# Performance work log

Hardware: AMD Instinct MI355X
Metric: run time of the kernel (lower is better)

## Reference

```python
import jax, jax.numpy as jnp
import numpy as np

NX, NY = 512, 512
FNUM, GNUM = 120, 120
NA = 1.35
WAVELENGTH = NX * NA / 100.0  # chosen so normalized period = 100
N_LIQUID = 1.44
M_RED = 0.25
LOW_LIGHT_THRES = 1e-3
SRC_STEEP = 8.0
RESIST_STEEP = 30.0
RESIST_INT = 0.225
DOSES = (0.98, 1.0, 1.02)
SRC_GRID = 13

X1 = NX // 2 - FNUM; X2 = NX // 2 + FNUM + 1
Y1 = NY // 2 - GNUM; Y2 = NY // 2 + GNUM + 1
_PER_X = NX / (WAVELENGTH / NA)
_PER_Y = NY / (WAVELENGTH / NA)
NORM_SPEC = _PER_X * _PER_Y
DFMDG = 1.0 / NORM_SPEC
_fm = (np.arange(X1, X2) - NX // 2) / _PER_X
_gm = (np.arange(Y1, Y2) - NY // 2) / _PER_Y
_FM, _GM = np.meshgrid(_fm, _gm)  # 'xy' indexing, shape [2*GNUM+1, 2*FNUM+1]
FM = jnp.asarray(_FM, jnp.float32)
GM = jnp.asarray(_GM, jnp.float32)


def cal_pupil(fg2):
    # obliquity factor; pupil phase is identically zero in this module
    num = 1.0 - (M_RED ** 2) * (NA ** 2) * fg2
    den = 1.0 - (NA / N_LIQUID) ** 2 * fg2
    return jnp.sqrt(jnp.sqrt(num / den))


def setup_inputs() -> dict:
    key = jax.random.key(0)
    g = np.linspace(-1.0, 1.0, SRC_GRID, dtype=np.float32)
    fxg, fyg = np.meshgrid(g, g)
    r = np.sqrt(fxg ** 2 + fyg ** 2)
    data = ((r >= 0.6) & (r <= 0.9)).astype(np.float32)  # annular source
    # sigmoid activation init: +1 where lit, -1 elsewhere (zeros, set 2 where data>0.5, sub 1)
    params = 2.0 * data - 1.0
    mask_value = jax.random.uniform(key, (NY, NX), jnp.float32)
    return {
        "mask_value": mask_value,
        "source_params": jnp.asarray(params, jnp.float32),
        "source_fx": jnp.asarray(fxg.reshape(-1), jnp.float32),
        "source_fy": jnp.asarray(fyg.reshape(-1), jnp.float32),
    }


def _forward(mask_value, source_params, source_fx, source_fy):
    # source activation + low-light pruning (masked_select expressed as zero-weighting)
    val = jax.nn.sigmoid(SRC_STEEP * source_params).reshape(-1)  # [S]
    valid = val >= LOW_LIGHT_THRES
    w = jnp.where(valid, val, 0.0)
    weight = jnp.sum(w)

    # normalization intensity (detached in the original)
    fxy2 = source_fx ** 2 + source_fy ** 2
    obl = cal_pupil(jnp.where(valid, fxy2, 0.0))
    norm_I = jax.lax.stop_gradient(
        N_LIQUID * DFMDG ** 2 * jnp.sum(w * (NORM_SPEC * obl) ** 2) / weight
    )

    # shifted pupil per source point over the mask frequency window
    F = FM[None, :, :] + source_fx[:, None, None]  # [S, Gy, Gx]
    G = GM[None, :, :] + source_fy[:, None, None]
    rho2 = F * F + G * G                            # == mask_fg2m + 2(fx*fm+fy*gm) + fxy2
    vmask = rho2 <= 1.0
    pupil = jnp.where(vmask, cal_pupil(jnp.where(vmask, rho2, 0.0)), 0.0)  # [S, Gy, Gx]

    S = w.shape[0]
    Is, Rs = [], []
    for d in DOSES:
        fv = jnp.fft.fftshift(jnp.fft.fft2(jnp.fft.ifftshift(mask_value * d)))
        win = fv[Y1:Y2, X1:X2]                      # [Gy, Gx] complex
        tempH = win[None, :, :] * pupil.astype(jnp.complex64)  # masked spectrum*pupil
        e = jnp.zeros((S, NY, NX), jnp.complex64).at[:, Y1:Y2, X1:X2].set(tempH)
        AA = jnp.fft.fftshift(jnp.fft.ifft2(e), axes=(-2, -1))
        I2 = AA.real ** 2 + AA.imag ** 2            # |AA * conj(AA)|
        intensity = jnp.einsum('s,syx->yx', w, I2) / weight / norm_I
        Is.append(intensity)
        Rs.append(jax.nn.sigmoid(RESIST_STEEP * (intensity - RESIST_INT)))
    # [2, 3, NY, NX]: [0] = aerial intensity per dose, [1] = resist image per dose
    return jnp.stack([jnp.stack(Is), jnp.stack(Rs)])


def reference(mask_value, source_params, source_fx, source_fy):
    return _forward(mask_value, source_params, source_fx, source_fy)
```

## Files before the change

### kernel.cpp

```cpp
#include <hip/hip_runtime.h>
#include <hip/hip_bf16.h>
#include <hip/hip_fp16.h>


#define SPLIT 8

static const size_t O_TW   = 4096;
static const size_t O_ACC  = 8192;
static const size_t ACC_BYTES = (size_t)SPLIT * 512 * 512 * 4;
static const size_t O_WIN  = O_ACC + ACC_BYTES;
static const size_t O_R1   = O_WIN + 464896;
static const size_t O_T2   = O_R1 + 987136;
static const size_t SLOT_BYTES = (size_t)512 * 244 * 4;

__device__ inline float2 cadd(float2 a, float2 b){ return make_float2(a.x+b.x, a.y+b.y); }
__device__ inline float2 csub(float2 a, float2 b){ return make_float2(a.x-b.x, a.y-b.y); }
__device__ inline float2 cmul(float2 a, float2 b){
  return make_float2(fmaf(a.x, b.x, -(a.y*b.y)), fmaf(a.x, b.y, a.y*b.x));
}
__device__ inline float2 twsgn(float2 t, int S) {
  return make_float2(t.x, (S > 0) ? t.y : -t.y);
}

template<int S, bool ZTOP>
__device__ inline void dft8(float2 v[8]) {
  const float sg = (float)S;
  const float C7 = 0.7071067811865476f;
  float2 t0, t1, t2, t3, t4, t5, t6, t7;
  if (ZTOP) {
    t0 = v[0]; t4 = v[0];
    t1 = v[1]; t5 = v[1];
    t2 = v[2]; t6 = v[2];
    t3 = v[3]; t7 = v[3];
  } else {
    t0=cadd(v[0],v[4]); t4=csub(v[0],v[4]);
    t1=cadd(v[1],v[5]); t5=csub(v[1],v[5]);
    t2=cadd(v[2],v[6]); t6=csub(v[2],v[6]);
    t3=cadd(v[3],v[7]); t7=csub(v[3],v[7]);
  }
  t5 = make_float2(C7*(t5.x - sg*t5.y), C7*(t5.y + sg*t5.x));
  t6 = make_float2(-sg*t6.y, sg*t6.x);
  t7 = make_float2(C7*(-t7.x - sg*t7.y), C7*(sg*t7.x - t7.y));
  float2 u0=cadd(t0,t2), u2=csub(t0,t2);
  float2 u1=cadd(t1,t3), u3=csub(t1,t3);
  u3 = make_float2(-sg*u3.y, sg*u3.x);
  float2 u4=cadd(t4,t6), u6=csub(t4,t6);
  float2 u5=cadd(t5,t7), u7=csub(t5,t7);
  u7 = make_float2(-sg*u7.y, sg*u7.x);
  v[0]=cadd(u0,u1); v[4]=csub(u0,u1);
  v[2]=cadd(u2,u3); v[6]=csub(u2,u3);
  v[1]=cadd(u4,u5); v[5]=csub(u4,u5);
  v[3]=cadd(u6,u7); v[7]=csub(u6,u7);
}

template<int S, bool ZTOP>
__device__ inline void wfft512(float2 v[8], int lane, float2* xch,
                               const float2* twt) {
  const int p2 = lane & 7, u0 = lane >> 3;
  dft8<S, ZTOP>(v);
  { float2 t1 = twsgn(twt[lane], S), acc = t1;
    v[1] = cmul(v[1], acc);
    #pragma unroll
    for (int u = 2; u < 8; u++) { acc = cmul(acc, t1); v[u] = cmul(v[u], acc); } }
  __builtin_amdgcn_wave_barrier();
  #pragma unroll
  for (int u = 0; u < 8; u++) xch[u*68 + p2*8 + u0] = v[u];
  __builtin_amdgcn_wave_barrier();
  { const float4* rp = (const float4*)(xch + u0*68 + p2*8);
    #pragma unroll
    for (int q = 0; q < 4; q++) {
      float4 t = rp[q];
      v[2*q]   = make_float2(t.x, t.y);
      v[2*q+1] = make_float2(t.z, t.w);
    } }
  dft8<S, false>(v);
  { float2 t1 = twsgn(twt[p2 << 3], S), acc = t1;
    v[1] = cmul(v[1], acc);
    #pragma unroll
    for (int u = 2; u < 8; u++) { acc = cmul(acc, t1); v[u] = cmul(v[u], acc); } }
  __builtin_amdgcn_wave_barrier();
  #pragma unroll
  for (int u = 0; u < 8; u++) xch[u*68 + lane] = v[u];
  __builtin_amdgcn_wave_barrier();
  { const float4* rp = (const float4*)(xch + p2*68 + u0*8);
    #pragma unroll
    for (int q = 0; q < 4; q++) {
      float4 t = rp[q];
      v[2*q]   = make_float2(t.x, t.y);
      v[2*q+1] = make_float2(t.z, t.w);
    } }
  dft8<S, false>(v);
}

__global__ void __launch_bounds__(256) k_setup(const float* prm, const float* sfx,
                                               const float* sfy, char* ws) {
  __shared__ float sw[169], sx[169], sy[169], scw[169];
  __shared__ double so[169];
  __shared__ int skeep[169];
  int t = threadIdx.x;
  if (t < 169) {
    float p = prm[t];
    float val = 1.f / (1.f + __expf(-8.f * p));
    float w = (val >= 0.001f) ? val : 0.f;
    double o = 0.0; float fx = 0.f, fy = 0.f;
    if (w > 0.f) {
      fx = sfx[t]; fy = sfy[t];
      double f2 = (double)fx*(double)fx + (double)fy*(double)fy;
      o = (double)w * sqrt((1.0 - 0.11390625 * f2) / (1.0 - 0.87890625 * f2));
    }
    sw[t] = w; so[t] = o; sx[t] = fx; sy[t] = fy;
  }
  float2* gtw = (float2*)(ws + O_TW);
  for (int k = t; k < 512; k += 256) {
    double a = 6.283185307179586476925286766559 * (double)k / 512.0;
    gtw[k] = make_float2((float)cos(a), (float)sin(a));
  }
  if (t < 241) ((float*)ws)[768 + t] = (float)(((double)(t - 120)) / 100.0);
  __syncthreads();
  if (t < 169) {
    float w = sw[t];
    int keep = 0; float cw = w;
    if (w > 0.f) {
      float fx = sx[t], fy = sy[t];
      int pr = -1;
      for (int s2 = 0; s2 < 169; s2++) {
        if (sw[s2] > 0.f && fabsf(sx[s2] + fx) < 1e-5f
                         && fabsf(sy[s2] + fy) < 1e-5f) { pr = s2; break; }
      }
      if (pr < 0 || pr == t) keep = 1;
      else if (pr > t) { keep = 1; cw = w + sw[pr]; }
    }
    skeep[t] = keep; scw[t] = cw;
  }
  __syncthreads();
  if (t == 0) {
    float* wsf = (float*)ws; int* wsi = (int*)ws;
    double Sden = 0.0; int c = 0;
    for (int s = 0; s < 169; s++) {
      Sden += so[s];
      if (skeep[s]) { wsf[64+c] = scw[s]; wsf[320+c] = sx[s]; wsf[576+c] = sy[s]; c++; }
    }
    wsi[0] = c;
    wsf[1] = (float)(1.0 / (262144.0 * 1.44 * Sden));
  }
}

__global__ void __launch_bounds__(256, 6) k_b1(const float* mask, const char* wsb,
                                               float2* R1t) {
  int lane = threadIdx.x & 63, wv = threadIdx.x >> 6;
  int y = blockIdx.x * 4 + wv;
  __shared__ __align__(16) float2 lds[4*544];
  __shared__ __align__(16) float2 twt[512];
  ((float4*)twt)[threadIdx.x] = ((const float4*)(wsb + O_TW))[threadIdx.x];
  __syncthreads();
  float2 v[8];
  #pragma unroll
  for (int q = 0; q < 8; q++) v[q] = make_float2(mask[y*512 + 64*q + lane], 0.f);
  wfft512<-1, false>(v, lane, lds + wv*544, twt);
  #pragma unroll
  for (int u = 0; u < 8; u++) {
    int k = (lane>>3) + 8*(lane&7) + 64*u;
    int beta = (k >= 392) ? (k - 392) : ((k <= 120) ? (k + 120) : -1);
    if (beta >= 0) R1t[beta*512 + y] = v[u];
  }
}

__global__ void __launch_bounds__(256, 6) k_b2(const float2* R1t, const char* wsb,
                                               float2* Wg) {
  int lane = threadIdx.x & 63, wv = threadIdx.x >> 6;
  int j = blockIdx.x * 4 + wv;
  __shared__ __align__(16) float2 lds[4*544];
  __shared__ __align__(16) float2 twt[512];
  ((float4*)twt)[threadIdx.x] = ((const float4*)(wsb + O_TW))[threadIdx.x];
  __syncthreads();
  float2 v[8];
  #pragma unroll
  for (int q = 0; q < 8; q++)
    v[q] = (j < 241) ? R1t[j*512 + 64*q + lane] : make_float2(0.f, 0.f);
  wfft512<-1, false>(v, lane, lds + wv*544, twt);
  if (j < 241) {
    #pragma unroll
    for (int u = 0; u < 8; u++) {
      int k = (lane>>3) + 8*(lane&7) + 64*u;
      int alpha = (k >= 392) ? (k - 392) : ((k <= 120) ? (k + 120) : -1);
      if (alpha >= 0) Wg[alpha*241 + j] = v[u];
    }
  }
}

__global__ void __launch_bounds__(256, 7) k_c1(const float2* Wg, const char* wsb,
                                               int base, __half2* T2) {
  const int*   cnt = (const int*)wsb;
  const float* wsf = (const float*)wsb;
  const float* FMt = (const float*)(wsb + 3072);
  int sic  = blockIdx.x / 31;
  int tile = blockIdx.x % 31;
  int slot = base + sic;
  if (slot >= *cnt) return;
  __shared__ __align__(16) float2 lds[4*544];
  __shared__ __align__(16) float2 twt[512];
  ((float4*)twt)[threadIdx.x] = ((const float4*)(wsb + O_TW))[threadIdx.x];
  __syncthreads();
  float fx = wsf[320 + slot], fy = wsf[576 + slot];
  float sqw = __fsqrt_rn(wsf[64 + slot]) * 0.001953125f;
  int lane = threadIdx.x & 63, wv = threadIdx.x >> 6;
  float2* xch = lds + wv*544;
  #pragma unroll
  for (int ph = 0; ph < 2; ph++) {
    int alpha = tile*8 + ph*4 + wv;
    bool arow = (alpha < 241);
    float Gf = __fadd_rn(arow ? FMt[alpha] : 0.f, fy);
    float g2 = __fmul_rn(Gf, Gf);
    bool active = arow && (g2 <= 1.0f);
    float2 v[8];
    #pragma unroll
    for (int q = 0; q < 8; q++) v[q] = make_float2(0.f, 0.f);
    if (active) {
      #pragma unroll
      for (int q = 0; q < 4; q++) {
        int n = 64*q + lane;
        if (n < 241) {
          float Ff = __fadd_rn(FMt[n], fx);
          float r2 = __fadd_rn(__fmul_rn(Ff, Ff), g2);
          if (r2 <= 1.0f) {
            float num = fmaf(-0.11390625f, r2, 1.0f);
            float den = fmaf(-0.87890625f, r2, 1.0f);
            float P = __fsqrt_rn(__fsqrt_rn(__fdividef(num, den))) * sqw;
            float2 Wv = Wg[alpha*241 + n];
            v[q] = make_float2(P * Wv.x, P * Wv.y);
          }
        }
      }
      wfft512<1, true>(v, lane, xch, twt);
    }
    #pragma unroll
    for (int u = 0; u < 8; u++) {
      int xx = (lane>>3) + 8*(lane&7) + 64*u;
      xch[xx] = v[u];
    }
    __syncthreads();
    int colb = tile*8 + ph*4;
    if (colb < 244) {
      #pragma unroll
      for (int r = 0; r < 2; r++) {
        int x = (int)threadIdx.x + 256*r;
        union { __half2 h[4]; float4 f; } u;
        #pragma unroll
        for (int wvi = 0; wvi < 4; wvi++) {
          float2 a = lds[wvi*544 + x];
          u.h[wvi] = __floats2half2_rn(a.x, a.y);
        }
        *(float4*)(T2 + ((size_t)sic*512 + x)*244 + colb) = u.f;
      }
    }
    __syncthreads();
  }
}

__global__ void __launch_bounds__(256, 7) k_c2(const __half2* T2, const char* wsb,
                                               int base, int CH, int first,
                                               float* accbuf) {
  const int* cnt = (const int*)wsb;
  int part = blockIdx.x & (SPLIT-1);
  int xg   = blockIdx.x >> 3;
  int lane = threadIdx.x & 63, wv = threadIdx.x >> 6;
  int x = xg*4 + wv;
  __shared__ __align__(16) float2 lds[4*544];
  __shared__ __align__(16) float2 twt[512];
  ((float4*)twt)[threadIdx.x] = ((const float4*)(wsb + O_TW))[threadIdx.x];
  __syncthreads();
  float2* xch = lds + wv*544;
  int count = *cnt;
  float av[8] = {0.f,0.f,0.f,0.f,0.f,0.f,0.f,0.f};
  int sic = part;
  bool act = (sic < CH) && (base + sic < count);
  __half2 pv[4] = {{0.f,0.f},{0.f,0.f},{0.f,0.f},{0.f,0.f}};
  if (act) {
    const __half2* row = T2 + ((size_t)sic*512 + x)*244;
    #pragma unroll
    for (int q = 0; q < 4; q++) {
      int n = 64*q + lane;
      pv[q] = (n < 241) ? row[n] : __half2{0.f, 0.f};
    }
  }
  while (act) {
    float2 v[8];
    #pragma unroll
    for (int q = 0; q < 4; q++) { float2 f = __half22float2(pv[q]); v[q] = f; }
    #pragma unroll
    for (int q = 4; q < 8; q++) v[q] = make_float2(0.f, 0.f);
    int nsic = sic + SPLIT;
    act = (nsic < CH) && (base + nsic < count);
    if (act) {
      const __half2* row = T2 + ((size_t)nsic*512 + x)*244;
      #pragma unroll
      for (int q = 0; q < 4; q++) {
        int n = 64*q + lane;
        pv[q] = (n < 241) ? row[n] : __half2{0.f, 0.f};
      }
    }
    wfft512<1, true>(v, lane, xch, twt);
    #pragma unroll
    for (int u = 0; u < 8; u++)
      av[u] += fmaf(v[u].x, v[u].x, v[u].y*v[u].y);
    sic = nsic;
  }
  float* a = accbuf + ((size_t)part << 18) + (size_t)x * 512;
  int y0 = (lane>>3) + 8*(lane&7);
  if (first) {
    #pragma unroll
    for (int u = 0; u < 8; u++) a[y0 + 64*u] = av[u];
  } else {
    #pragma unroll
    for (int u = 0; u < 8; u++) a[y0 + 64*u] += av[u];
  }
}

__global__ void __launch_bounds__(256) k_final(const float* acc, const char* wsb,
                                               float* out) {
  __shared__ float tile[64][65];
  const float* wsf = (const float*)wsb;
  float scale = wsf[1];
  int x0 = (blockIdx.x & 7) * 64, y0 = (blockIdx.x >> 3) * 64;
  int j = threadIdx.x & 63, i0 = threadIdx.x >> 6;
  #pragma unroll
  for (int k = 0; k < 16; k++) {
    int i = i0 + 4*k;
    const float* ap = acc + (size_t)(x0 + i)*512 + y0 + j;
    float s = 0.f;
    #pragma unroll
    for (int p = 0; p < SPLIT; p++) s += ap[(size_t)p << 18];
    tile[i][j] = s;
  }
  __syncthreads();
  const float dd[3] = {0.9604f, 1.0f, 1.0404f};
  #pragma unroll
  for (int k = 0; k < 16; k++) {
    int yy = i0 + 4*k;
    float I = scale * tile[j][yy];
    int o = (y0 + yy)*512 + x0 + j;
    #pragma unroll
    for (int d = 0; d < 3; d++) {
      float Ik = dd[d] * I;
      out[(size_t)d*262144 + o] = Ik;
      out[(size_t)(3+d)*262144 + o] = 1.f / (1.f + __expf(-30.f*(Ik - 0.225f)));
    }
  }
}

extern "C" void kernel_launch(void* const* d_in, const int* in_sizes, int n_in,
                              void* d_out, int out_size, void* d_ws, size_t ws_size,
                              hipStream_t stream) {
  (void)in_sizes; (void)n_in; (void)out_size;
  const float* mask = (const float*)d_in[0];
  const float* prm  = (const float*)d_in[1];
  const float* sfx  = (const float*)d_in[2];
  const float* sfy  = (const float*)d_in[3];
  float* out = (float*)d_out;
  char*  ws  = (char*)d_ws;

  float*   acc = (float*)(ws + O_ACC);
  float2*  Wg  = (float2*)(ws + O_WIN);
  float2*  R1t = (float2*)(ws + O_R1);
  __half2* T2  = (__half2*)(ws + O_T2);

  k_setup<<<dim3(1),   dim3(256), 0, stream>>>(prm, sfx, sfy, ws);
  k_b1  <<<dim3(128), dim3(256), 0, stream>>>(mask, (const char*)ws, R1t);
  k_b2  <<<dim3(61),  dim3(256), 0, stream>>>(R1t, (const char*)ws, Wg);

  size_t avail = (ws_size > O_T2) ? (ws_size - O_T2) : 0;
  int CH = (int)(avail / SLOT_BYTES);
  if (CH > 169) CH = 169;
  if (CH < 1)   CH = 1;
  for (int base = 0; base < 169; base += CH) {
    k_c1<<<dim3((unsigned)(CH*31)),  dim3(256), 0, stream>>>(Wg, (const char*)ws, base, T2);
    k_c2<<<dim3(128*SPLIT),          dim3(256), 0, stream>>>(T2, (const char*)ws, base, CH,
                                                             (base == 0) ? 1 : 0, acc);
  }
  k_final<<<dim3(64), dim3(256), 0, stream>>>(acc, (const char*)ws, out);
}
```

Baseline: 138.3 us.

## Fuse all stages into one persistent kernel with software grid barriers

Replaces the chain of setup, row FFT, column FFT, per-source pupil FFT, accumulate and finalize kernels with a single persistent kernel of 512 blocks. Stages are separated by an atomic-counter grid barrier, which removes launch overhead and inter-kernel gaps. The c2 stage now maps one block per column with four waves splitting sources (SPLIT reduced to 4). The CH chunking that depended on workspace size is dropped, so all source slots must fit in the workspace at once. Correctness depends on all 512 blocks being co-resident; if they are not, the spin barrier can deadlock. Also, fewer blocks work in the early stages and c2 parallelism changes.

```diff
diff --git a/kernel.cpp b/kernel.cpp
--- a/kernel.cpp
+++ b/kernel.cpp
@@ -3,9 +3,10 @@
 #include <hip/hip_fp16.h>
 
 
-#define SPLIT 8
-
-static const size_t O_TW   = 4096;
+#define NBLK 512
+#define SPLIT 4
+
+static const size_t O_BAR  = 2048;
 static const size_t O_ACC  = 8192;
 static const size_t ACC_BYTES = (size_t)SPLIT * 512 * 512 * 4;
 static const size_t O_WIN  = O_ACC + ACC_BYTES;
@@ -20,6 +21,19 @@
 }
 __device__ inline float2 twsgn(float2 t, int S) {
   return make_float2(t.x, (S > 0) ? t.y : -t.y);
+}
+
+__device__ inline void gridbar(int* cnt, int gen) {
+  __syncthreads();
+  if (threadIdx.x == 0) {
+    __threadfence();
+    atomicAdd(cnt, 1);
+    int target = (gen + 1) * NBLK;
+    while (__hip_atomic_load(cnt, __ATOMIC_ACQUIRE, __HIP_MEMORY_SCOPE_AGENT) < target)
+      __builtin_amdgcn_s_sleep(2);
+    __threadfence();
+  }
+  __syncthreads();
 }
 
 template<int S, bool ZTOP>
@@ -92,258 +106,244 @@
   dft8<S, false>(v);
 }
 
-__global__ void __launch_bounds__(256) k_setup(const float* prm, const float* sfx,
-                                               const float* sfy, char* ws) {
-  __shared__ float sw[169], sx[169], sy[169], scw[169];
-  __shared__ double so[169];
-  __shared__ int skeep[169];
-  int t = threadIdx.x;
-  if (t < 169) {
-    float p = prm[t];
-    float val = 1.f / (1.f + __expf(-8.f * p));
-    float w = (val >= 0.001f) ? val : 0.f;
-    double o = 0.0; float fx = 0.f, fy = 0.f;
-    if (w > 0.f) {
-      fx = sfx[t]; fy = sfy[t];
-      double f2 = (double)fx*(double)fx + (double)fy*(double)fy;
-      o = (double)w * sqrt((1.0 - 0.11390625 * f2) / (1.0 - 0.87890625 * f2));
-    }
-    sw[t] = w; so[t] = o; sx[t] = fx; sy[t] = fy;
-  }
-  float2* gtw = (float2*)(ws + O_TW);
+#define ARENA_BYTES (4096 + 17408 + 1024)
+
+__global__ void __launch_bounds__(256, 2)
+k_fused(const float* __restrict__ mask, const float* __restrict__ prm,
+        const float* __restrict__ sfx, const float* __restrict__ sfy,
+        char* __restrict__ ws, float* __restrict__ out) {
+  __shared__ __align__(16) char arena[ARENA_BYTES];
+  float2* twt = (float2*)arena;
+  float2* lds = (float2*)(arena + 4096);
+  float*  FMt = (float*)(arena + 4096 + 17408);
+  int*    bar = (int*)(ws + O_BAR);
+  float*  wsf = (float*)ws;
+  int t = threadIdx.x, lane = t & 63, wv = t >> 6, b = blockIdx.x;
+
+  float*   acc = (float*)(ws + O_ACC);
+  float2*  Wg  = (float2*)(ws + O_WIN);
+  float2*  R1t = (float2*)(ws + O_R1);
+  __half2* T2  = (__half2*)(ws + O_T2);
+
   for (int k = t; k < 512; k += 256) {
     double a = 6.283185307179586476925286766559 * (double)k / 512.0;
-    gtw[k] = make_float2((float)cos(a), (float)sin(a));
-  }
-  if (t < 241) ((float*)ws)[768 + t] = (float)(((double)(t - 120)) / 100.0);
-  __syncthreads();
-  if (t < 169) {
-    float w = sw[t];
-    int keep = 0; float cw = w;
-    if (w > 0.f) {
-      float fx = sx[t], fy = sy[t];
-      int pr = -1;
-      for (int s2 = 0; s2 < 169; s2++) {
-        if (sw[s2] > 0.f && fabsf(sx[s2] + fx) < 1e-5f
-                         && fabsf(sy[s2] + fy) < 1e-5f) { pr = s2; break; }
-      }
-      if (pr < 0 || pr == t) keep = 1;
-      else if (pr > t) { keep = 1; cw = w + sw[pr]; }
-    }
-    skeep[t] = keep; scw[t] = cw;
-  }
-  __syncthreads();
-  if (t == 0) {
-    float* wsf = (float*)ws; int* wsi = (int*)ws;
-    double Sden = 0.0; int c = 0;
-    for (int s = 0; s < 169; s++) {
-      Sden += so[s];
-      if (skeep[s]) { wsf[64+c] = scw[s]; wsf[320+c] = sx[s]; wsf[576+c] = sy[s]; c++; }
-    }
-    wsi[0] = c;
-    wsf[1] = (float)(1.0 / (262144.0 * 1.44 * Sden));
-  }
-}
-
-__global__ void __launch_bounds__(256, 6) k_b1(const float* mask, const char* wsb,
-                                               float2* R1t) {
-  int lane = threadIdx.x & 63, wv = threadIdx.x >> 6;
-  int y = blockIdx.x * 4 + wv;
-  __shared__ __align__(16) float2 lds[4*544];
-  __shared__ __align__(16) float2 twt[512];
-  ((float4*)twt)[threadIdx.x] = ((const float4*)(wsb + O_TW))[threadIdx.x];
-  __syncthreads();
-  float2 v[8];
-  #pragma unroll
-  for (int q = 0; q < 8; q++) v[q] = make_float2(mask[y*512 + 64*q + lane], 0.f);
-  wfft512<-1, false>(v, lane, lds + wv*544, twt);
-  #pragma unroll
-  for (int u = 0; u < 8; u++) {
-    int k = (lane>>3) + 8*(lane&7) + 64*u;
-    int beta = (k >= 392) ? (k - 392) : ((k <= 120) ? (k + 120) : -1);
-    if (beta >= 0) R1t[beta*512 + y] = v[u];
-  }
-}
-
-__global__ void __launch_bounds__(256, 6) k_b2(const float2* R1t, const char* wsb,
-                                               float2* Wg) {
-  int lane = threadIdx.x & 63, wv = threadIdx.x >> 6;
-  int j = blockIdx.x * 4 + wv;
-  __shared__ __align__(16) float2 lds[4*544];
-  __shared__ __align__(16) float2 twt[512];
-  ((float4*)twt)[threadIdx.x] = ((const float4*)(wsb + O_TW))[threadIdx.x];
-  __syncthreads();
-  float2 v[8];
-  #pragma unroll
-  for (int q = 0; q < 8; q++)
-    v[q] = (j < 241) ? R1t[j*512 + 64*q + lane] : make_float2(0.f, 0.f);
-  wfft512<-1, false>(v, lane, lds + wv*544, twt);
-  if (j < 241) {
+    twt[k] = make_float2((float)cos(a), (float)sin(a));
+  }
+  if (t < 241) FMt[t] = (float)(((double)(t - 120)) / 100.0);
+
+  if (b == 0) {
+    float*  sw   = (float*)(arena + 4096);
+    float*  sx_  = sw + 192;
+    float*  sy_  = sx_ + 192;
+    float*  scw  = sy_ + 192;
+    double* so   = (double*)(arena + 4096 + 3072);
+    int*    skp  = (int*)(arena + 4096 + 3072 + 1408);
+    if (t < 169) {
+      float p = prm[t];
+      float val = 1.f / (1.f + __expf(-8.f * p));
+      float w = (val >= 0.001f) ? val : 0.f;
+      double o = 0.0; float fx = 0.f, fy = 0.f;
+      if (w > 0.f) {
+        fx = sfx[t]; fy = sfy[t];
+        double f2 = (double)fx*(double)fx + (double)fy*(double)fy;
+        o = (double)w * sqrt((1.0 - 0.11390625 * f2) / (1.0 - 0.87890625 * f2));
+      }
+      sw[t] = w; so[t] = o; sx_[t] = fx; sy_[t] = fy;
+    }
+    __syncthreads();
+    if (t < 169) {
+      float w = sw[t];
+      int keep = 0; float cw = w;
+      if (w > 0.f) {
+        float fx = sx_[t], fy = sy_[t];
+        int pr = -1;
+        for (int s2 = 0; s2 < 169; s2++) {
+          if (sw[s2] > 0.f && fabsf(sx_[s2] + fx) < 1e-5f
+                           && fabsf(sy_[s2] + fy) < 1e-5f) { pr = s2; break; }
+        }
+        if (pr < 0 || pr == t) keep = 1;
+        else if (pr > t) { keep = 1; cw = w + sw[pr]; }
+      }
+      skp[t] = keep; scw[t] = cw;
+    }
+    __syncthreads();
+    if (t == 0) {
+      double Sden = 0.0; int c = 0;
+      for (int s = 0; s < 169; s++) {
+        Sden += so[s];
+        if (skp[s]) { wsf[64+c] = scw[s]; wsf[320+c] = sx_[s]; wsf[576+c] = sy_[s]; c++; }
+      }
+      ((int*)ws)[0] = c;
+      wsf[1] = (float)(1.0 / (262144.0 * 1.44 * Sden));
+    }
+  }
+  gridbar(bar, 0);
+
+  if (b < 128) {
+    int y = b * 4 + wv;
+    float2 v[8];
+    #pragma unroll
+    for (int q = 0; q < 8; q++) v[q] = make_float2(mask[y*512 + 64*q + lane], 0.f);
+    wfft512<-1, false>(v, lane, lds + wv*544, twt);
     #pragma unroll
     for (int u = 0; u < 8; u++) {
       int k = (lane>>3) + 8*(lane&7) + 64*u;
-      int alpha = (k >= 392) ? (k - 392) : ((k <= 120) ? (k + 120) : -1);
-      if (alpha >= 0) Wg[alpha*241 + j] = v[u];
-    }
-  }
-}
-
-__global__ void __launch_bounds__(256, 7) k_c1(const float2* Wg, const char* wsb,
-                                               int base, __half2* T2) {
-  const int*   cnt = (const int*)wsb;
-  const float* wsf = (const float*)wsb;
-  const float* FMt = (const float*)(wsb + 3072);
-  int sic  = blockIdx.x / 31;
-  int tile = blockIdx.x % 31;
-  int slot = base + sic;
-  if (slot >= *cnt) return;
-  __shared__ __align__(16) float2 lds[4*544];
-  __shared__ __align__(16) float2 twt[512];
-  ((float4*)twt)[threadIdx.x] = ((const float4*)(wsb + O_TW))[threadIdx.x];
-  __syncthreads();
-  float fx = wsf[320 + slot], fy = wsf[576 + slot];
-  float sqw = __fsqrt_rn(wsf[64 + slot]) * 0.001953125f;
-  int lane = threadIdx.x & 63, wv = threadIdx.x >> 6;
-  float2* xch = lds + wv*544;
-  #pragma unroll
-  for (int ph = 0; ph < 2; ph++) {
-    int alpha = tile*8 + ph*4 + wv;
-    bool arow = (alpha < 241);
-    float Gf = __fadd_rn(arow ? FMt[alpha] : 0.f, fy);
-    float g2 = __fmul_rn(Gf, Gf);
-    bool active = arow && (g2 <= 1.0f);
+      int beta = (k >= 392) ? (k - 392) : ((k <= 120) ? (k + 120) : -1);
+      if (beta >= 0) R1t[beta*512 + y] = v[u];
+    }
+  }
+  gridbar(bar, 1);
+
+  if (b < 61) {
+    int j = b * 4 + wv;
     float2 v[8];
     #pragma unroll
-    for (int q = 0; q < 8; q++) v[q] = make_float2(0.f, 0.f);
-    if (active) {
-      #pragma unroll
-      for (int q = 0; q < 4; q++) {
-        int n = 64*q + lane;
-        if (n < 241) {
-          float Ff = __fadd_rn(FMt[n], fx);
-          float r2 = __fadd_rn(__fmul_rn(Ff, Ff), g2);
-          if (r2 <= 1.0f) {
-            float num = fmaf(-0.11390625f, r2, 1.0f);
-            float den = fmaf(-0.87890625f, r2, 1.0f);
-            float P = __fsqrt_rn(__fsqrt_rn(__fdividef(num, den))) * sqw;
-            float2 Wv = Wg[alpha*241 + n];
-            v[q] = make_float2(P * Wv.x, P * Wv.y);
+    for (int q = 0; q < 8; q++)
+      v[q] = (j < 241) ? R1t[j*512 + 64*q + lane] : make_float2(0.f, 0.f);
+    wfft512<-1, false>(v, lane, lds + wv*544, twt);
+    if (j < 241) {
+      #pragma unroll
+      for (int u = 0; u < 8; u++) {
+        int k = (lane>>3) + 8*(lane&7) + 64*u;
+        int alpha = (k >= 392) ? (k - 392) : ((k <= 120) ? (k + 120) : -1);
+        if (alpha >= 0) Wg[alpha*241 + j] = v[u];
+      }
+    }
+  }
+  gridbar(bar, 2);
+
+  int count = *(volatile int*)ws;
+
+  for (int task = b; task < count * 31; task += NBLK) {
+    int sic  = task / 31;
+    int tile = task % 31;
+    float fx = wsf[320 + sic], fy = wsf[576 + sic];
+    float sqw = __fsqrt_rn(wsf[64 + sic]) * 0.001953125f;
+    float2* xch = lds + wv*544;
+    #pragma unroll
+    for (int ph = 0; ph < 2; ph++) {
+      int alpha = tile*8 + ph*4 + wv;
+      bool arow = (alpha < 241);
+      float Gf = __fadd_rn(arow ? FMt[alpha] : 0.f, fy);
+      float g2 = __fmul_rn(Gf, Gf);
+      bool active = arow && (g2 <= 1.0f);
+      float2 v[8];
+      #pragma unroll
+      for (int q = 0; q < 8; q++) v[q] = make_float2(0.f, 0.f);
+      if (active) {
+        #pragma unroll
+        for (int q = 0; q < 4; q++) {
+          int n = 64*q + lane;
+          if (n < 241) {
+            float Ff = __fadd_rn(FMt[n], fx);
+            float r2 = __fadd_rn(__fmul_rn(Ff, Ff), g2);
+            if (r2 <= 1.0f) {
+              float num = fmaf(-0.11390625f, r2, 1.0f);
+              float den = fmaf(-0.87890625f, r2, 1.0f);
+              float P = __fsqrt_rn(__fsqrt_rn(__fdividef(num, den))) * sqw;
+              float2 Wv = Wg[alpha*241 + n];
+              v[q] = make_float2(P * Wv.x, P * Wv.y);
+            }
           }
         }
-      }
-      wfft512<1, true>(v, lane, xch, twt);
-    }
-    #pragma unroll
-    for (int u = 0; u < 8; u++) {
-      int xx = (lane>>3) + 8*(lane&7) + 64*u;
-      xch[xx] = v[u];
-    }
-    __syncthreads();
-    int colb = tile*8 + ph*4;
-    if (colb < 244) {
-      #pragma unroll
-      for (int r = 0; r < 2; r++) {
-        int x = (int)threadIdx.x + 256*r;
-        union { __half2 h[4]; float4 f; } u;
+        wfft512<1, true>(v, lane, xch, twt);
+      }
+      #pragma unroll
+      for (int u = 0; u < 8; u++) {
+        int xx = (lane>>3) + 8*(lane&7) + 64*u;
+        xch[xx] = v[u];
+      }
+      __syncthreads();
+      int colb = tile*8 + ph*4;
+      if (colb < 244) {
         #pragma unroll
-        for (int wvi = 0; wvi < 4; wvi++) {
-          float2 a = lds[wvi*544 + x];
-          u.h[wvi] = __floats2half2_rn(a.x, a.y);
+        for (int r = 0; r < 2; r++) {
+          int x = t + 256*r;
+          union { __half2 h[4]; float4 f; } u;
+          #pragma unroll
+          for (int wvi = 0; wvi < 4; wvi++) {
+            float2 a = lds[wvi*544 + x];
+            u.h[wvi] = __floats2half2_rn(a.x, a.y);
+          }
+          *(float4*)(T2 + ((size_t)sic*512 + x)*244 + colb) = u.f;
         }
-        *(float4*)(T2 + ((size_t)sic*512 + x)*244 + colb) = u.f;
-      }
-    }
-    __syncthreads();
-  }
-}
-
-__global__ void __launch_bounds__(256, 7) k_c2(const __half2* T2, const char* wsb,
-                                               int base, int CH, int first,
-                                               float* accbuf) {
-  const int* cnt = (const int*)wsb;
-  int part = blockIdx.x & (SPLIT-1);
-  int xg   = blockIdx.x >> 3;
-  int lane = threadIdx.x & 63, wv = threadIdx.x >> 6;
-  int x = xg*4 + wv;
-  __shared__ __align__(16) float2 lds[4*544];
-  __shared__ __align__(16) float2 twt[512];
-  ((float4*)twt)[threadIdx.x] = ((const float4*)(wsb + O_TW))[threadIdx.x];
-  __syncthreads();
-  float2* xch = lds + wv*544;
-  int count = *cnt;
-  float av[8] = {0.f,0.f,0.f,0.f,0.f,0.f,0.f,0.f};
-  int sic = part;
-  bool act = (sic < CH) && (base + sic < count);
-  __half2 pv[4] = {{0.f,0.f},{0.f,0.f},{0.f,0.f},{0.f,0.f}};
-  if (act) {
-    const __half2* row = T2 + ((size_t)sic*512 + x)*244;
-    #pragma unroll
-    for (int q = 0; q < 4; q++) {
-      int n = 64*q + lane;
-      pv[q] = (n < 241) ? row[n] : __half2{0.f, 0.f};
-    }
-  }
-  while (act) {
-    float2 v[8];
-    #pragma unroll
-    for (int q = 0; q < 4; q++) { float2 f = __half22float2(pv[q]); v[q] = f; }
-    #pragma unroll
-    for (int q = 4; q < 8; q++) v[q] = make_float2(0.f, 0.f);
-    int nsic = sic + SPLIT;
-    act = (nsic < CH) && (base + nsic < count);
+      }
+      __syncthreads();
+    }
+  }
+  gridbar(bar, 3);
+
+  {
+    int x = b;
+    float2* xch = lds + wv*544;
+    float av[8] = {0.f,0.f,0.f,0.f,0.f,0.f,0.f,0.f};
+    int sic = wv;
+    bool act = (sic < count);
+    __half2 pv[4] = {{0.f,0.f},{0.f,0.f},{0.f,0.f},{0.f,0.f}};
     if (act) {
-      const __half2* row = T2 + ((size_t)nsic*512 + x)*244;
+      const __half2* row = T2 + ((size_t)sic*512 + x)*244;
       #pragma unroll
       for (int q = 0; q < 4; q++) {
         int n = 64*q + lane;
         pv[q] = (n < 241) ? row[n] : __half2{0.f, 0.f};
       }
     }
-    wfft512<1, true>(v, lane, xch, twt);
-    #pragma unroll
-    for (int u = 0; u < 8; u++)
-      av[u] += fmaf(v[u].x, v[u].x, v[u].y*v[u].y);
-    sic = nsic;
-  }
-  float* a = accbuf + ((size_t)part << 18) + (size_t)x * 512;
-  int y0 = (lane>>3) + 8*(lane&7);
-  if (first) {
+    while (act) {
+      float2 v[8];
+      #pragma unroll
+      for (int q = 0; q < 4; q++) { float2 f = __half22float2(pv[q]); v[q] = f; }
+      #pragma unroll
+      for (int q = 4; q < 8; q++) v[q] = make_float2(0.f, 0.f);
+      int nsic = sic + SPLIT;
+      act = (nsic < count);
+      if (act) {
+        const __half2* row = T2 + ((size_t)nsic*512 + x)*244;
+        #pragma unroll
+        for (int q = 0; q < 4; q++) {
+          int n = 64*q + lane;
+          pv[q] = (n < 241) ? row[n] : __half2{0.f, 0.f};
+        }
+      }
+      wfft512<1, true>(v, lane, xch, twt);
+      #pragma unroll
+      for (int u = 0; u < 8; u++)
+        av[u] += fmaf(v[u].x, v[u].x, v[u].y*v[u].y);
+      sic = nsic;
+    }
+    float* a = acc + ((size_t)wv << 18) + (size_t)x * 512;
+    int y0 = (lane>>3) + 8*(lane&7);
     #pragma unroll
     for (int u = 0; u < 8; u++) a[y0 + 64*u] = av[u];
-  } else {
-    #pragma unroll
-    for (int u = 0; u < 8; u++) a[y0 + 64*u] += av[u];
-  }
-}
-
-__global__ void __launch_bounds__(256) k_final(const float* acc, const char* wsb,
-                                               float* out) {
-  __shared__ float tile[64][65];
-  const float* wsf = (const float*)wsb;
-  float scale = wsf[1];
-  int x0 = (blockIdx.x & 7) * 64, y0 = (blockIdx.x >> 3) * 64;
-  int j = threadIdx.x & 63, i0 = threadIdx.x >> 6;
-  #pragma unroll
-  for (int k = 0; k < 16; k++) {
-    int i = i0 + 4*k;
-    const float* ap = acc + (size_t)(x0 + i)*512 + y0 + j;
-    float s = 0.f;
-    #pragma unroll
-    for (int p = 0; p < SPLIT; p++) s += ap[(size_t)p << 18];
-    tile[i][j] = s;
-  }
-  __syncthreads();
-  const float dd[3] = {0.9604f, 1.0f, 1.0404f};
-  #pragma unroll
-  for (int k = 0; k < 16; k++) {
-    int yy = i0 + 4*k;
-    float I = scale * tile[j][yy];
-    int o = (y0 + yy)*512 + x0 + j;
-    #pragma unroll
-    for (int d = 0; d < 3; d++) {
-      float Ik = dd[d] * I;
-      out[(size_t)d*262144 + o] = Ik;
-      out[(size_t)(3+d)*262144 + o] = 1.f / (1.f + __expf(-30.f*(Ik - 0.225f)));
+  }
+  gridbar(bar, 4);
+
+  if (b < 64) {
+    float (*tile)[65] = (float (*)[65])lds;
+    float scale = wsf[1];
+    int x0 = (b & 7) * 64, y0 = (b >> 3) * 64;
+    int j = lane, i0 = wv;
+    #pragma unroll
+    for (int k = 0; k < 16; k++) {
+      int i = i0 + 4*k;
+      const float* ap = acc + (size_t)(x0 + i)*512 + y0 + j;
+      float s = 0.f;
+      #pragma unroll
+      for (int p = 0; p < SPLIT; p++) s += ap[(size_t)p << 18];
+      tile[i][j] = s;
+    }
+    __syncthreads();
+    const float dd[3] = {0.9604f, 1.0f, 1.0404f};
+    #pragma unroll
+    for (int k = 0; k < 16; k++) {
+      int yy = i0 + 4*k;
+      float I = scale * tile[j][yy];
+      int o = (y0 + yy)*512 + x0 + j;
+      #pragma unroll
+      for (int d = 0; d < 3; d++) {
+        float Ik = dd[d] * I;
+        out[(size_t)d*262144 + o] = Ik;
+        out[(size_t)(3+d)*262144 + o] = 1.f / (1.f + __expf(-30.f*(Ik - 0.225f)));
+      }
     }
   }
 }
@@ -351,31 +351,13 @@
 extern "C" void kernel_launch(void* const* d_in, const int* in_sizes, int n_in,
                               void* d_out, int out_size, void* d_ws, size_t ws_size,
                               hipStream_t stream) {
-  (void)in_sizes; (void)n_in; (void)out_size;
+  (void)in_sizes; (void)n_in; (void)out_size; (void)ws_size;
   const float* mask = (const float*)d_in[0];
   const float* prm  = (const float*)d_in[1];
   const float* sfx  = (const float*)d_in[2];
   const float* sfy  = (const float*)d_in[3];
-  float* out = (float*)d_out;
-  char*  ws  = (char*)d_ws;
-
-  float*   acc = (float*)(ws + O_ACC);
-  float2*  Wg  = (float2*)(ws + O_WIN);
-  float2*  R1t = (float2*)(ws + O_R1);
-  __half2* T2  = (__half2*)(ws + O_T2);
-
-  k_setup<<<dim3(1),   dim3(256), 0, stream>>>(prm, sfx, sfy, ws);
-  k_b1  <<<dim3(128), dim3(256), 0, stream>>>(mask, (const char*)ws, R1t);
-  k_b2  <<<dim3(61),  dim3(256), 0, stream>>>(R1t, (const char*)ws, Wg);
-
-  size_t avail = (ws_size > O_T2) ? (ws_size - O_T2) : 0;
-  int CH = (int)(avail / SLOT_BYTES);
-  if (CH > 169) CH = 169;
-  if (CH < 1)   CH = 1;
-  for (int base = 0; base < 169; base += CH) {
-    k_c1<<<dim3((unsigned)(CH*31)),  dim3(256), 0, stream>>>(Wg, (const char*)ws, base, T2);
-    k_c2<<<dim3(128*SPLIT),          dim3(256), 0, stream>>>(T2, (const char*)ws, base, CH,
-                                                             (base == 0) ? 1 : 0, acc);
-  }
-  k_final<<<dim3(64), dim3(256), 0, stream>>>(acc, (const char*)ws, out);
-}
+  char* ws = (char*)d_ws;
+  hipMemsetAsync(ws + O_BAR, 0, 64, stream);
+  k_fused<<<dim3(NBLK), dim3(256), 0, stream>>>(mask, prm, sfx, sfy, ws,
+                                                (float*)d_out);
+}
```

Result: slower. 445.8 us (+222.3%).

## Fold setup into first FFT kernel and make k_c1 a persistent grid

Applied to the files above, without the earlier changes.

Removes the separate single-block setup kernel by running the source-weight and normalisation logic in block 0 of k_b1. Every kernel now builds its twiddle table in shared memory with double-precision cos/sin instead of loading it from workspace. k_c1 becomes a fixed 1024-block grid that loops over the tasks of the active source slots, with the frequency table also kept in shared memory. This saves one launch and avoids launching blocks that would exit early, but the per-block double-precision trig adds compute to every block.

```diff
diff --git a/kernel.cpp b/kernel.cpp
--- a/kernel.cpp
+++ b/kernel.cpp
@@ -5,7 +5,6 @@
 
 #define SPLIT 8
 
-static const size_t O_TW   = 4096;
 static const size_t O_ACC  = 8192;
 static const size_t ACC_BYTES = (size_t)SPLIT * 512 * 512 * 4;
 static const size_t O_WIN  = O_ACC + ACC_BYTES;
@@ -20,6 +19,13 @@
 }
 __device__ inline float2 twsgn(float2 t, int S) {
   return make_float2(t.x, (S > 0) ? t.y : -t.y);
+}
+
+__device__ inline void build_twt(float2* twt) {
+  for (int k = (int)threadIdx.x; k < 512; k += 256) {
+    double a = 6.283185307179586476925286766559 * (double)k / 512.0;
+    twt[k] = make_float2((float)cos(a), (float)sin(a));
+  }
 }
 
 template<int S, bool ZTOP>
@@ -92,67 +98,60 @@
   dft8<S, false>(v);
 }
 
-__global__ void __launch_bounds__(256) k_setup(const float* prm, const float* sfx,
-                                               const float* sfy, char* ws) {
-  __shared__ float sw[169], sx[169], sy[169], scw[169];
-  __shared__ double so[169];
-  __shared__ int skeep[169];
-  int t = threadIdx.x;
-  if (t < 169) {
-    float p = prm[t];
-    float val = 1.f / (1.f + __expf(-8.f * p));
-    float w = (val >= 0.001f) ? val : 0.f;
-    double o = 0.0; float fx = 0.f, fy = 0.f;
-    if (w > 0.f) {
-      fx = sfx[t]; fy = sfy[t];
-      double f2 = (double)fx*(double)fx + (double)fy*(double)fy;
-      o = (double)w * sqrt((1.0 - 0.11390625 * f2) / (1.0 - 0.87890625 * f2));
-    }
-    sw[t] = w; so[t] = o; sx[t] = fx; sy[t] = fy;
-  }
-  float2* gtw = (float2*)(ws + O_TW);
-  for (int k = t; k < 512; k += 256) {
-    double a = 6.283185307179586476925286766559 * (double)k / 512.0;
-    gtw[k] = make_float2((float)cos(a), (float)sin(a));
-  }
-  if (t < 241) ((float*)ws)[768 + t] = (float)(((double)(t - 120)) / 100.0);
-  __syncthreads();
-  if (t < 169) {
-    float w = sw[t];
-    int keep = 0; float cw = w;
-    if (w > 0.f) {
-      float fx = sx[t], fy = sy[t];
-      int pr = -1;
-      for (int s2 = 0; s2 < 169; s2++) {
-        if (sw[s2] > 0.f && fabsf(sx[s2] + fx) < 1e-5f
-                         && fabsf(sy[s2] + fy) < 1e-5f) { pr = s2; break; }
-      }
-      if (pr < 0 || pr == t) keep = 1;
-      else if (pr > t) { keep = 1; cw = w + sw[pr]; }
-    }
-    skeep[t] = keep; scw[t] = cw;
-  }
-  __syncthreads();
-  if (t == 0) {
-    float* wsf = (float*)ws; int* wsi = (int*)ws;
-    double Sden = 0.0; int c = 0;
-    for (int s = 0; s < 169; s++) {
-      Sden += so[s];
-      if (skeep[s]) { wsf[64+c] = scw[s]; wsf[320+c] = sx[s]; wsf[576+c] = sy[s]; c++; }
-    }
-    wsi[0] = c;
-    wsf[1] = (float)(1.0 / (262144.0 * 1.44 * Sden));
-  }
-}
-
-__global__ void __launch_bounds__(256, 6) k_b1(const float* mask, const char* wsb,
-                                               float2* R1t) {
-  int lane = threadIdx.x & 63, wv = threadIdx.x >> 6;
-  int y = blockIdx.x * 4 + wv;
+__global__ void __launch_bounds__(256, 6) k_b1(const float* mask, const float* prm,
+                                               const float* sfx, const float* sfy,
+                                               char* ws, float2* R1t) {
+  int t = threadIdx.x, lane = t & 63, wv = t >> 6;
   __shared__ __align__(16) float2 lds[4*544];
   __shared__ __align__(16) float2 twt[512];
-  ((float4*)twt)[threadIdx.x] = ((const float4*)(wsb + O_TW))[threadIdx.x];
-  __syncthreads();
+  build_twt(twt);
+  if (blockIdx.x == 0) {
+    float*  sw  = (float*)lds;
+    float*  sxx = sw + 192; float* syy = sxx + 192; float* scw = syy + 192;
+    double* so  = (double*)(sw + 768);
+    int*    skp = (int*)(so + 176);
+    if (t < 169) {
+      float p = prm[t];
+      float val = 1.f / (1.f + __expf(-8.f * p));
+      float w = (val >= 0.001f) ? val : 0.f;
+      double o = 0.0; float fx = 0.f, fy = 0.f;
+      if (w > 0.f) {
+        fx = sfx[t]; fy = sfy[t];
+        double f2 = (double)fx*(double)fx + (double)fy*(double)fy;
+        o = (double)w * sqrt((1.0 - 0.11390625 * f2) / (1.0 - 0.87890625 * f2));
+      }
+      sw[t] = w; so[t] = o; sxx[t] = fx; syy[t] = fy;
+    }
+    __syncthreads();
+    if (t < 169) {
+      float w = sw[t];
+      int keep = 0; float cw = w;
+      if (w > 0.f) {
+        float fx = sxx[t], fy = syy[t];
+        int pr = -1;
+        for (int s2 = 0; s2 < 169; s2++) {
+          if (sw[s2] > 0.f && fabsf(sxx[s2] + fx) < 1e-5f
+                           && fabsf(syy[s2] + fy) < 1e-5f) { pr = s2; break; }
+        }
+        if (pr < 0 || pr == t) keep = 1;
+        else if (pr > t) { keep = 1; cw = w + sw[pr]; }
+      }
+      skp[t] = keep; scw[t] = cw;
+    }
+    __syncthreads();
+    if (t == 0) {
+      float* wsf = (float*)ws;
+      double Sden = 0.0; int c = 0;
+      for (int s = 0; s < 169; s++) {
+        Sden += so[s];
+        if (skp[s]) { wsf[64+c] = scw[s]; wsf[320+c] = sxx[s]; wsf[576+c] = syy[s]; c++; }
+      }
+      ((int*)ws)[0] = c;
+      wsf[1] = (float)(1.0 / (262144.0 * 1.44 * Sden));
+    }
+  }
+  __syncthreads();
+  int y = blockIdx.x * 4 + wv;
   float2 v[8];
   #pragma unroll
   for (int q = 0; q < 8; q++) v[q] = make_float2(mask[y*512 + 64*q + lane], 0.f);
@@ -165,13 +164,12 @@
   }
 }
 
-__global__ void __launch_bounds__(256, 6) k_b2(const float2* R1t, const char* wsb,
-                                               float2* Wg) {
+__global__ void __launch_bounds__(256, 6) k_b2(const float2* R1t, float2* Wg) {
   int lane = threadIdx.x & 63, wv = threadIdx.x >> 6;
   int j = blockIdx.x * 4 + wv;
   __shared__ __align__(16) float2 lds[4*544];
   __shared__ __align__(16) float2 twt[512];
-  ((float4*)twt)[threadIdx.x] = ((const float4*)(wsb + O_TW))[threadIdx.x];
+  build_twt(twt);
   __syncthreads();
   float2 v[8];
   #pragma unroll
@@ -189,71 +187,76 @@
 }
 
 __global__ void __launch_bounds__(256, 7) k_c1(const float2* Wg, const char* wsb,
-                                               int base, __half2* T2) {
-  const int*   cnt = (const int*)wsb;
+                                               int base, int CH, __half2* T2) {
   const float* wsf = (const float*)wsb;
-  const float* FMt = (const float*)(wsb + 3072);
-  int sic  = blockIdx.x / 31;
-  int tile = blockIdx.x % 31;
-  int slot = base + sic;
-  if (slot >= *cnt) return;
   __shared__ __align__(16) float2 lds[4*544];
   __shared__ __align__(16) float2 twt[512];
-  ((float4*)twt)[threadIdx.x] = ((const float4*)(wsb + O_TW))[threadIdx.x];
-  __syncthreads();
-  float fx = wsf[320 + slot], fy = wsf[576 + slot];
-  float sqw = __fsqrt_rn(wsf[64 + slot]) * 0.001953125f;
+  __shared__ float FMt[241];
+  build_twt(twt);
+  if (threadIdx.x < 241)
+    FMt[threadIdx.x] = (float)(((double)((int)threadIdx.x - 120)) / 100.0);
+  __syncthreads();
+  int active = *(const int*)wsb - base;
+  if (active > CH) active = CH;
+  int ntask = active * 31;
   int lane = threadIdx.x & 63, wv = threadIdx.x >> 6;
   float2* xch = lds + wv*544;
-  #pragma unroll
-  for (int ph = 0; ph < 2; ph++) {
-    int alpha = tile*8 + ph*4 + wv;
-    bool arow = (alpha < 241);
-    float Gf = __fadd_rn(arow ? FMt[alpha] : 0.f, fy);
-    float g2 = __fmul_rn(Gf, Gf);
-    bool active = arow && (g2 <= 1.0f);
-    float2 v[8];
-    #pragma unroll
-    for (int q = 0; q < 8; q++) v[q] = make_float2(0.f, 0.f);
-    if (active) {
+  for (int task = (int)blockIdx.x; task < ntask; task += (int)gridDim.x) {
+    int sic  = task / 31;
+    int tile = task % 31;
+    int slot = base + sic;
+    float fx = wsf[320 + slot], fy = wsf[576 + slot];
+    float sqw = __fsqrt_rn(wsf[64 + slot]) * 0.001953125f;
+    #pragma unroll
+    for (int ph = 0; ph < 2; ph++) {
+      int alpha = tile*8 + ph*4 + wv;
+      bool arow = (alpha < 241);
+      float Gf = __fadd_rn(arow ? FMt[alpha] : 0.f, fy);
+      float g2 = __fmul_rn(Gf, Gf);
+      bool active_row = arow && (g2 <= 1.0f);
+      float2 v[8];
       #pragma unroll
-      for (int q = 0; q < 4; q++) {
-        int n = 64*q + lane;
-        if (n < 241) {
-          float Ff = __fadd_rn(FMt[n], fx);
-          float r2 = __fadd_rn(__fmul_rn(Ff, Ff), g2);
-          if (r2 <= 1.0f) {
-            float num = fmaf(-0.11390625f, r2, 1.0f);
-            float den = fmaf(-0.87890625f, r2, 1.0f);
-            float P = __fsqrt_rn(__fsqrt_rn(__fdividef(num, den))) * sqw;
-            float2 Wv = Wg[alpha*241 + n];
-            v[q] = make_float2(P * Wv.x, P * Wv.y);
+      for (int q = 0; q < 8; q++) v[q] = make_float2(0.f, 0.f);
+      if (active_row) {
+        #pragma unroll
+        for (int q = 0; q < 4; q++) {
+          int n = 64*q + lane;
+          if (n < 241) {
+            float Ff = __fadd_rn(FMt[n], fx);
+            float r2 = __fadd_rn(__fmul_rn(Ff, Ff), g2);
+            if (r2 <= 1.0f) {
+              float num = fmaf(-0.11390625f, r2, 1.0f);
+              float den = fmaf(-0.87890625f, r2, 1.0f);
+              float P = __fsqrt_rn(__fsqrt_rn(__fdividef(num, den))) * sqw;
+              float2 Wv = Wg[alpha*241 + n];
+              v[q] = make_float2(P * Wv.x, P * Wv.y);
+            }
           }
         }
-      }
-      wfft512<1, true>(v, lane, xch, twt);
-    }
-    #pragma unroll
-    for (int u = 0; u < 8; u++) {
-      int xx = (lane>>3) + 8*(lane&7) + 64*u;
-      xch[xx] = v[u];
-    }
-    __syncthreads();
-    int colb = tile*8 + ph*4;
-    if (colb < 244) {
+        wfft512<1, true>(v, lane, xch, twt);
+      }
       #pragma unroll
-      for (int r = 0; r < 2; r++) {
-        int x = (int)threadIdx.x + 256*r;
-        union { __half2 h[4]; float4 f; } u;
+      for (int u = 0; u < 8; u++) {
+        int xx = (lane>>3) + 8*(lane&7) + 64*u;
+        xch[xx] = v[u];
+      }
+      __syncthreads();
+      int colb = tile*8 + ph*4;
+      if (colb < 244) {
         #pragma unroll
-        for (int wvi = 0; wvi < 4; wvi++) {
-          float2 a = lds[wvi*544 + x];
-          u.h[wvi] = __floats2half2_rn(a.x, a.y);
+        for (int r = 0; r < 2; r++) {
+          int x = (int)threadIdx.x + 256*r;
+          union { __half2 h[4]; float4 f; } u;
+          #pragma unroll
+          for (int wvi = 0; wvi < 4; wvi++) {
+            float2 a = lds[wvi*544 + x];
+            u.h[wvi] = __floats2half2_rn(a.x, a.y);
+          }
+          *(float4*)(T2 + ((size_t)sic*512 + x)*244 + colb) = u.f;
         }
-        *(float4*)(T2 + ((size_t)sic*512 + x)*244 + colb) = u.f;
-      }
-    }
-    __syncthreads();
+      }
+      __syncthreads();
+    }
   }
 }
 
@@ -267,7 +270,7 @@
   int x = xg*4 + wv;
   __shared__ __align__(16) float2 lds[4*544];
   __shared__ __align__(16) float2 twt[512];
-  ((float4*)twt)[threadIdx.x] = ((const float4*)(wsb + O_TW))[threadIdx.x];
+  build_twt(twt);
   __syncthreads();
   float2* xch = lds + wv*544;
   int count = *cnt;
@@ -364,18 +367,17 @@
   float2*  R1t = (float2*)(ws + O_R1);
   __half2* T2  = (__half2*)(ws + O_T2);
 
-  k_setup<<<dim3(1),   dim3(256), 0, stream>>>(prm, sfx, sfy, ws);
-  k_b1  <<<dim3(128), dim3(256), 0, stream>>>(mask, (const char*)ws, R1t);
-  k_b2  <<<dim3(61),  dim3(256), 0, stream>>>(R1t, (const char*)ws, Wg);
+  k_b1<<<dim3(128), dim3(256), 0, stream>>>(mask, prm, sfx, sfy, ws, R1t);
+  k_b2<<<dim3(61),  dim3(256), 0, stream>>>(R1t, Wg);
 
   size_t avail = (ws_size > O_T2) ? (ws_size - O_T2) : 0;
   int CH = (int)(avail / SLOT_BYTES);
   if (CH > 169) CH = 169;
   if (CH < 1)   CH = 1;
   for (int base = 0; base < 169; base += CH) {
-    k_c1<<<dim3((unsigned)(CH*31)),  dim3(256), 0, stream>>>(Wg, (const char*)ws, base, T2);
-    k_c2<<<dim3(128*SPLIT),          dim3(256), 0, stream>>>(T2, (const char*)ws, base, CH,
-                                                             (base == 0) ? 1 : 0, acc);
+    k_c1<<<dim3(1024),      dim3(256), 0, stream>>>(Wg, (const char*)ws, base, CH, T2);
+    k_c2<<<dim3(128*SPLIT), dim3(256), 0, stream>>>(T2, (const char*)ws, base, CH,
+                                                    (base == 0) ? 1 : 0, acc);
   }
   k_final<<<dim3(64), dim3(256), 0, stream>>>(acc, (const char*)ws, out);
 }
```

Measured after the change: 138.2 us. Within noise of the previous version (-0.1%).
